# Kernel tuning notes

Hardware: AMD Instinct MI355X
Metric: run time of the kernel (lower is better)

## Reference

```python
import jax, jax.numpy as jnp
import numpy as np

N = 50000        # nodes
DEG = 32         # in-degree per node
E = N * DEG      # edges
T = 4            # towers
NODE = 128       # node_dim
OUT = 128        # out_dim
IN_T = NODE // T   # 32, divide_input tower slice
OUT_T = OUT // T   # 32
AVG_D_LOG = float(np.log(5.0))  # avg_d = {'log': log(4+1)}
EPS = 1e-5


def setup_inputs() -> dict:
    key = jax.random.key(0)
    ks = jax.random.split(key, 6)
    h = jax.random.normal(ks[0], (N, NODE), jnp.float32)
    src = jax.random.randint(ks[1], (E,), 0, N)
    # every node gets exactly DEG incoming edges (sorted dst)
    dst = jnp.repeat(jnp.arange(N), DEG)
    # per-tower pretrans MLP (1 layer): Linear(2*IN_T -> OUT_T)
    W_pre = jax.random.normal(ks[2], (T, 2 * IN_T, OUT_T), jnp.float32) * 0.05
    b_pre = jnp.zeros((T, OUT_T), jnp.float32)
    # per-tower posttrans MLP (1 layer): Linear(12*OUT_T + IN_T -> OUT_T)
    W_post = jax.random.normal(ks[3], (T, 12 * OUT_T + IN_T, OUT_T), jnp.float32) * 0.05
    b_post = jnp.zeros((T, OUT_T), jnp.float32)
    # mixing network: Linear(OUT -> OUT) + LeakyReLU
    W_mix = jax.random.normal(ks[4], (OUT, OUT), jnp.float32) * 0.05
    b_mix = jnp.zeros((OUT,), jnp.float32)
    return dict(h=h, src=src, dst=dst, W_pre=W_pre, b_pre=b_pre,
                W_post=W_post, b_post=b_post, W_mix=W_mix, b_mix=b_mix)


def _pna_forward(h, src, dst, W_pre, b_pre, W_post, b_post, W_mix, b_mix):
    ht = h.reshape(N, T, IN_T)                    # divide_input: tower slices
    z2 = jnp.concatenate([ht[src], ht[dst]], axis=-1)   # [E,T,2*IN_T] (src||dst)
    # pretrans: MLP(1 layer) then ReLU
    e = jax.nn.relu(jnp.einsum('etk,tko->eto', z2, W_pre) + b_pre)  # [E,T,OUT_T]

    deg = jax.ops.segment_sum(jnp.ones((E,), h.dtype), dst, num_segments=N)  # [N]
    deg_c = jnp.maximum(deg, 1.0)[:, None, None]
    seg = lambda x: jax.ops.segment_sum(x, dst, num_segments=N)
    mean = seg(e) / deg_c                          # [N,T,OUT_T]
    mean_sq = seg(e * e) / deg_c
    std = jnp.sqrt(jax.nn.relu(mean_sq - mean * mean) + EPS)
    mx = jax.ops.segment_max(e, dst, num_segments=N)
    mn = jax.ops.segment_min(e, dst, num_segments=N)
    agg = jnp.concatenate([mean, mx, mn, std], axis=-1)   # [N,T,4*OUT_T]

    # scalers: identity, amplification, attenuation (D = in-degree)
    sc = jnp.log(deg + 1.0) / AVG_D_LOG            # [N]
    amp = agg * sc[:, None, None]
    att = agg / jnp.maximum(sc, EPS)[:, None, None]
    h_agg = jnp.concatenate([agg, amp, att], axis=-1)     # [N,T,12*OUT_T]

    # posttrans: cat(h_tower, aggregated) -> MLP(1 layer) -> ReLU
    z = jnp.concatenate([ht, h_agg], axis=-1)      # [N,T,IN_T+12*OUT_T]
    hp = jax.nn.relu(jnp.einsum('ntk,tko->nto', z, W_post) + b_post)  # [N,T,OUT_T]
    h_cat = hp.reshape(N, OUT)

    h_out = jax.nn.leaky_relu(h_cat @ W_mix + b_mix, 0.01)
    return h + h_out                               # residual (node_dim == out_dim)


def reference(h, src, dst, W_pre, b_pre, W_post, b_post, W_mix, b_mix):
    return _pna_forward(h, src, dst, W_pre, b_pre, W_post, b_post, W_mix, b_mix)
```

## Files before the change

kernel.cpp:

```cpp
#include <hip/hip_runtime.h>
#include <hip/hip_bf16.h>
#include <math.h>

#define N_NODES 50000
#define DEG     32
#define NBF     16
#define EPSV    1e-5f

typedef __attribute__((ext_vector_type(8))) short short8;
typedef __attribute__((ext_vector_type(4))) float f32x4;
typedef __attribute__((ext_vector_type(2))) float f32x2;

__global__ void k_prep(const float* __restrict__ W_post, const float* __restrict__ W_mix,
                       const float* __restrict__ W_pre,
                       __hip_bfloat16* __restrict__ WeffT, __hip_bfloat16* __restrict__ WmixT,
                       __hip_bfloat16* __restrict__ WpreT, float sc, float isc) {
    int i = blockIdx.x * 256 + threadIdx.x;
    if (i < 20480) {
        int k = i % 160, to = i / 160, o = to & 31, t = to >> 5;
        const float* Wt = W_post + t * 416 * 32;
        float v;
        if (k < 32) v = Wt[k * 32 + o];
        else {
            int g = k - 32;
            v = Wt[(32 + g) * 32 + o] + sc * Wt[(160 + g) * 32 + o] + isc * Wt[(288 + g) * 32 + o];
        }
        WeffT[i] = __float2bfloat16(v);
    } else if (i < 36864) {
        int j = i - 20480;
        int k = j & 127, o = j >> 7;
        WmixT[j] = __float2bfloat16(W_mix[k * 128 + o]);
    } else if (i < 45056) {
        int q = i - 36864;
        int k = q & 31, o = (q >> 5) & 31, p = q >> 10;
        int t = p >> 1, half = p & 1;
        WpreT[q] = __float2bfloat16(W_pre[t * 2048 + (half * 32 + k) * 32 + o]);
    }
}

__global__ __launch_bounds__(256) void k_proj(const float* __restrict__ h,
        const __hip_bfloat16* __restrict__ WpreT, const float* __restrict__ b_pre,
        __hip_bfloat16* __restrict__ Pd, __hip_bfloat16* __restrict__ Ps) {
    __shared__ __align__(16) __hip_bfloat16 sA[64][136];
    int tid = threadIdx.x, w = tid >> 6, lane = tid & 63;
    int nb = blockIdx.x * 64;

    int colc = (tid & 31) * 4, rowb = tid >> 5;
#pragma unroll
    for (int i = 0; i < 8; ++i) {
        int row = i * 8 + rowb;
        int n = nb + row;
        unsigned int lo = 0, hi = 0;
        if (n < N_NODES) {
            float4 f = *(const float4*)(h + n * 128 + colc);
            lo = (unsigned int)__bfloat16_as_ushort(__float2bfloat16(f.x)) |
                 ((unsigned int)__bfloat16_as_ushort(__float2bfloat16(f.y)) << 16);
            hi = (unsigned int)__bfloat16_as_ushort(__float2bfloat16(f.z)) |
                 ((unsigned int)__bfloat16_as_ushort(__float2bfloat16(f.w)) << 16);
        }
        *(uint2*)(&sA[row][colc]) = make_uint2(lo, hi);
    }
    __syncthreads();

    int col = lane & 15, quad = lane >> 4;
    int r0 = w * 16;
    short8 a[4];
#pragma unroll
    for (int t = 0; t < 4; ++t)
        a[t] = *(const short8*)(&sA[r0 + col][t * 32 + quad * 8]);

#pragma unroll
    for (int p = 0; p < 8; ++p) {
        int t = p >> 1, isPd = p & 1;
#pragma unroll
        for (int ct = 0; ct < 2; ++ct) {
            int o = ct * 16 + col;
            short8 b = *(const short8*)(WpreT + p * 1024 + o * 32 + quad * 8);
            f32x4 acc = {0.f, 0.f, 0.f, 0.f};
            acc = __builtin_amdgcn_mfma_f32_16x16x32_bf16(a[t], b, acc, 0, 0, 0);
            float bp = isPd ? b_pre[t * 32 + o] : 0.f;
            __hip_bfloat16* dst = (isPd ? Pd : Ps);
#pragma unroll
            for (int r = 0; r < 4; ++r) {
                int n = nb + r0 + quad * 4 + r;
                if (n < N_NODES)
                    dst[n * 128 + t * 32 + o] = __float2bfloat16(acc[r] + bp);
            }
        }
    }
}

__global__ __launch_bounds__(256) void k_fused(const float* __restrict__ h,
        const int* __restrict__ src, const __hip_bfloat16* __restrict__ Pd,
        const __hip_bfloat16* __restrict__ Ps, const __hip_bfloat16* __restrict__ WeffT,
        const __hip_bfloat16* __restrict__ WmixT, const float* __restrict__ b_post,
        const float* __restrict__ b_mix, float* __restrict__ out) {
    __shared__ __align__(16) __hip_bfloat16 sZ[NBF][648];
    __shared__ __align__(16) __hip_bfloat16 sHp[NBF][136];
    int tid = threadIdx.x, w = tid >> 6, lane = tid & 63;
    int nb = blockIdx.x * NBF;

    int c0 = 2 * lane;
    int tA = c0 >> 5, oA = c0 & 31;
    const f32x2 zero2 = {0.f, 0.f};
#pragma unroll
    for (int r = 0; r < 4; ++r) {
        int row = r * 4 + w;
        int n = nb + row;
        int vsrc = src[n * DEG + (lane & 31)];
        float2 hv = *(const float2*)(h + n * 128 + c0);
        unsigned int pdu = *(const unsigned int*)(Pd + n * 128 + c0);
        f32x2 pd2 = {__uint_as_float(pdu << 16), __uint_as_float(pdu & 0xffff0000u)};
        f32x2 sum = zero2, sq = zero2;
        f32x2 mx = {-1e30f, -1e30f}, mn = {1e30f, 1e30f};
#pragma unroll
        for (int j0 = 0; j0 < DEG; j0 += 16) {
            unsigned int pv[16];
#pragma unroll
            for (int u = 0; u < 16; ++u) {
                int s = __builtin_amdgcn_readlane(vsrc, j0 + u);
                pv[u] = *(const unsigned int*)(Ps + s * 128 + c0);
            }
#pragma unroll
            for (int u = 0; u < 16; ++u) {
                f32x2 f = {__uint_as_float(pv[u] << 16),
                           __uint_as_float(pv[u] & 0xffff0000u)};
                f32x2 e = __builtin_elementwise_max(f + pd2, zero2);
                sum += e;
                sq = e * e + sq;
                mx = __builtin_elementwise_max(mx, e);
                mn = __builtin_elementwise_min(mn, e);
            }
        }
        f32x2 mean = sum * (1.f / DEG);
        f32x2 var = sq * (1.f / DEG) - mean * mean;
        float sd0 = sqrtf(fmaxf(var.x, 0.f) + EPSV);
        float sd1 = sqrtf(fmaxf(var.y, 0.f) + EPSV);
        unsigned int* zr = (unsigned int*)(&sZ[row][tA * 160 + oA]);
        auto pack = [](float a, float b) {
            return (unsigned int)(__bfloat16_as_ushort(__float2bfloat16(a))) |
                   ((unsigned int)(__bfloat16_as_ushort(__float2bfloat16(b))) << 16);
        };
        zr[0]  = pack(hv.x, hv.y);
        zr[16] = pack(mean.x, mean.y);
        zr[32] = pack(mx.x, mx.y);
        zr[48] = pack(mn.x, mn.y);
        zr[64] = pack(sd0, sd1);
    }
    __syncthreads();

    int col = lane & 15, quad = lane >> 4;
#pragma unroll
    for (int i = 0; i < 2; ++i) {
        int ct = w * 2 + i, t = ct >> 1, nt = ct & 1;
        f32x4 acc = {0.f, 0.f, 0.f, 0.f};
        int oc = t * 32 + nt * 16 + col;
        const __hip_bfloat16* wrow = WeffT + oc * 160 + quad * 8;
#pragma unroll
        for (int ks = 0; ks < 5; ++ks) {
            short8 a = *(const short8*)(&sZ[col][t * 160 + ks * 32 + quad * 8]);
            short8 b = *(const short8*)(wrow + ks * 32);
            acc = __builtin_amdgcn_mfma_f32_16x16x32_bf16(a, b, acc, 0, 0, 0);
        }
        float bp = b_post[oc];
#pragma unroll
        for (int r = 0; r < 4; ++r)
            sHp[quad * 4 + r][oc] = __float2bfloat16(fmaxf(acc[r] + bp, 0.f));
    }
    __syncthreads();

#pragma unroll
    for (int i = 0; i < 2; ++i) {
        int nt = w * 2 + i;
        f32x4 acc = {0.f, 0.f, 0.f, 0.f};
        int oc = nt * 16 + col;
        const __hip_bfloat16* wrow = WmixT + oc * 128 + quad * 8;
#pragma unroll
        for (int ks = 0; ks < 4; ++ks) {
            short8 a = *(const short8*)(&sHp[col][ks * 32 + quad * 8]);
            short8 b = *(const short8*)(wrow + ks * 32);
            acc = __builtin_amdgcn_mfma_f32_16x16x32_bf16(a, b, acc, 0, 0, 0);
        }
        float bm = b_mix[oc];
#pragma unroll
        for (int r = 0; r < 4; ++r) {
            int n = nb + quad * 4 + r;
            float m = acc[r] + bm;
            m = m > 0.f ? m : 0.01f * m;
            out[n * 128 + oc] = h[n * 128 + oc] + m;
        }
    }
}

extern "C" void kernel_launch(void* const* d_in, const int* in_sizes, int n_in,
                              void* d_out, int out_size, void* d_ws, size_t ws_size,
                              hipStream_t stream) {
    const float* h      = (const float*)d_in[0];
    const int*   src    = (const int*)d_in[1];
    const float* W_pre  = (const float*)d_in[3];
    const float* b_pre  = (const float*)d_in[4];
    const float* W_post = (const float*)d_in[5];
    const float* b_post = (const float*)d_in[6];
    const float* W_mix  = (const float*)d_in[7];
    const float* b_mix  = (const float*)d_in[8];
    float* out = (float*)d_out;

    char* ws = (char*)d_ws;
    __hip_bfloat16* WeffT = (__hip_bfloat16*)ws;
    __hip_bfloat16* WmixT = (__hip_bfloat16*)(ws + 40960);
    __hip_bfloat16* WpreT = (__hip_bfloat16*)(ws + 73728);
    __hip_bfloat16* Pd    = (__hip_bfloat16*)(ws + 90112);
    __hip_bfloat16* Ps    = (__hip_bfloat16*)(ws + 90112 + 12800000);

    double scd = log(33.0) / log(5.0);
    float sc = (float)scd, isc = (float)(1.0 / scd);

    hipLaunchKernelGGL(k_prep, dim3(176), dim3(256), 0, stream,
                       W_post, W_mix, W_pre, WeffT, WmixT, WpreT, sc, isc);
    hipLaunchKernelGGL(k_proj, dim3((N_NODES + 63) / 64), dim3(256), 0, stream,
                       h, WpreT, b_pre, Pd, Ps);
    hipLaunchKernelGGL(k_fused, dim3(N_NODES / NBF), dim3(256), 0, stream,
                       h, src, Pd, Ps, WeffT, WmixT, b_post, b_mix, out);
}
```

Measured before the change: 171.6 us.

## Switch edge projections to fp16 with packed half aggregation, fold prep into proj

Stores the per-node projections Pd and Ps as fp16 instead of bf16 and runs the edge aggregation (add, relu, sum, sum of squares, max, min) with packed half2 arithmetic. Each lane now covers four channels, so the neighbour gather is 8 bytes per load and half the lanes serve a second node. The separate weight-prep launch is folded into the projection kernel, which now converts W_pre on the fly and writes its output through shared memory as coalesced 16-byte stores. The aim is fewer launches, fewer ALU instructions per edge and wider memory transactions, at the cost of accumulating sums and squares in fp16, which can lose precision or overflow.

```diff
diff --git a/kernel.cpp b/kernel.cpp
--- a/kernel.cpp
+++ b/kernel.cpp
@@ -1,5 +1,6 @@
 #include <hip/hip_runtime.h>
 #include <hip/hip_bf16.h>
+#include <hip/hip_fp16.h>
 #include <math.h>
 
 #define N_NODES 50000
@@ -9,90 +10,103 @@
 
 typedef __attribute__((ext_vector_type(8))) short short8;
 typedef __attribute__((ext_vector_type(4))) float f32x4;
-typedef __attribute__((ext_vector_type(2))) float f32x2;
-
-__global__ void k_prep(const float* __restrict__ W_post, const float* __restrict__ W_mix,
-                       const float* __restrict__ W_pre,
-                       __hip_bfloat16* __restrict__ WeffT, __hip_bfloat16* __restrict__ WmixT,
-                       __hip_bfloat16* __restrict__ WpreT, float sc, float isc) {
-    int i = blockIdx.x * 256 + threadIdx.x;
-    if (i < 20480) {
-        int k = i % 160, to = i / 160, o = to & 31, t = to >> 5;
-        const float* Wt = W_post + t * 416 * 32;
-        float v;
-        if (k < 32) v = Wt[k * 32 + o];
-        else {
-            int g = k - 32;
-            v = Wt[(32 + g) * 32 + o] + sc * Wt[(160 + g) * 32 + o] + isc * Wt[(288 + g) * 32 + o];
-        }
-        WeffT[i] = __float2bfloat16(v);
-    } else if (i < 36864) {
-        int j = i - 20480;
-        int k = j & 127, o = j >> 7;
-        WmixT[j] = __float2bfloat16(W_mix[k * 128 + o]);
-    } else if (i < 45056) {
-        int q = i - 36864;
-        int k = q & 31, o = (q >> 5) & 31, p = q >> 10;
-        int t = p >> 1, half = p & 1;
-        WpreT[q] = __float2bfloat16(W_pre[t * 2048 + (half * 32 + k) * 32 + o]);
-    }
+typedef __attribute__((ext_vector_type(2))) _Float16 h16x2;
+typedef __attribute__((ext_vector_type(4))) unsigned int uint4v;
+
+__device__ __forceinline__ unsigned int bfpack(float a, float b) {
+    return (unsigned int)__bfloat16_as_ushort(__float2bfloat16(a)) |
+           ((unsigned int)__bfloat16_as_ushort(__float2bfloat16(b)) << 16);
 }
 
 __global__ __launch_bounds__(256) void k_proj(const float* __restrict__ h,
-        const __hip_bfloat16* __restrict__ WpreT, const float* __restrict__ b_pre,
-        __hip_bfloat16* __restrict__ Pd, __hip_bfloat16* __restrict__ Ps) {
-    __shared__ __align__(16) __hip_bfloat16 sA[64][136];
+        const float* __restrict__ W_pre, const float* __restrict__ b_pre,
+        const float* __restrict__ W_post, const float* __restrict__ W_mix,
+        __hip_bfloat16* __restrict__ WeffT, __hip_bfloat16* __restrict__ WmixT,
+        _Float16* __restrict__ Pd, _Float16* __restrict__ Ps, float sc, float isc) {
     int tid = threadIdx.x, w = tid >> 6, lane = tid & 63;
     int nb = blockIdx.x * 64;
 
+    if (blockIdx.x < 144) {
+        int i = blockIdx.x * 256 + tid;
+        if (i < 20480) {
+            int k = i % 160, to = i / 160, o = to & 31, t = to >> 5;
+            const float* Wt = W_post + t * 416 * 32;
+            float v;
+            if (k < 32) v = Wt[k * 32 + o];
+            else {
+                int g = k - 32;
+                v = Wt[(32 + g) * 32 + o] + sc * Wt[(160 + g) * 32 + o]
+                  + isc * Wt[(288 + g) * 32 + o];
+            }
+            WeffT[i] = __float2bfloat16(v);
+        } else {
+            int j = i - 20480;
+            int k = j & 127, o = j >> 7;
+            WmixT[j] = __float2bfloat16(W_mix[k * 128 + o]);
+        }
+    }
+
+    __shared__ __align__(16) __hip_bfloat16 sA[64][136];
     int colc = (tid & 31) * 4, rowb = tid >> 5;
 #pragma unroll
     for (int i = 0; i < 8; ++i) {
-        int row = i * 8 + rowb;
-        int n = nb + row;
+        int row = i * 8 + rowb, n = nb + row;
         unsigned int lo = 0, hi = 0;
         if (n < N_NODES) {
             float4 f = *(const float4*)(h + n * 128 + colc);
-            lo = (unsigned int)__bfloat16_as_ushort(__float2bfloat16(f.x)) |
-                 ((unsigned int)__bfloat16_as_ushort(__float2bfloat16(f.y)) << 16);
-            hi = (unsigned int)__bfloat16_as_ushort(__float2bfloat16(f.z)) |
-                 ((unsigned int)__bfloat16_as_ushort(__float2bfloat16(f.w)) << 16);
+            lo = bfpack(f.x, f.y); hi = bfpack(f.z, f.w);
         }
         *(uint2*)(&sA[row][colc]) = make_uint2(lo, hi);
     }
     __syncthreads();
-
-    int col = lane & 15, quad = lane >> 4;
-    int r0 = w * 16;
+    int col = lane & 15, quad = lane >> 4, r0 = w * 16;
     short8 a[4];
 #pragma unroll
     for (int t = 0; t < 4; ++t)
         a[t] = *(const short8*)(&sA[r0 + col][t * 32 + quad * 8]);
-
-#pragma unroll
-    for (int p = 0; p < 8; ++p) {
-        int t = p >> 1, isPd = p & 1;
-#pragma unroll
-        for (int ct = 0; ct < 2; ++ct) {
-            int o = ct * 16 + col;
-            short8 b = *(const short8*)(WpreT + p * 1024 + o * 32 + quad * 8);
-            f32x4 acc = {0.f, 0.f, 0.f, 0.f};
-            acc = __builtin_amdgcn_mfma_f32_16x16x32_bf16(a[t], b, acc, 0, 0, 0);
-            float bp = isPd ? b_pre[t * 32 + o] : 0.f;
-            __hip_bfloat16* dst = (isPd ? Pd : Ps);
-#pragma unroll
-            for (int r = 0; r < 4; ++r) {
-                int n = nb + r0 + quad * 4 + r;
-                if (n < N_NODES)
-                    dst[n * 128 + t * 32 + o] = __float2bfloat16(acc[r] + bp);
-            }
-        }
+    __syncthreads();
+    unsigned short* sOut = (unsigned short*)sA;
+
+#pragma unroll
+    for (int half = 0; half < 2; ++half) {
+#pragma unroll
+        for (int t = 0; t < 4; ++t) {
+#pragma unroll
+            for (int ct = 0; ct < 2; ++ct) {
+                int o = ct * 16 + col;
+                const float* wp = W_pre + t * 2048 + (half * 32 + quad * 8) * 32 + o;
+                unsigned int bw0 = bfpack(wp[0],   wp[32]);
+                unsigned int bw1 = bfpack(wp[64],  wp[96]);
+                unsigned int bw2 = bfpack(wp[128], wp[160]);
+                unsigned int bw3 = bfpack(wp[192], wp[224]);
+                uint4v bwv = {bw0, bw1, bw2, bw3};
+                short8 b = __builtin_bit_cast(short8, bwv);
+                f32x4 acc = {0.f, 0.f, 0.f, 0.f};
+                acc = __builtin_amdgcn_mfma_f32_16x16x32_bf16(a[t], b, acc, 0, 0, 0);
+                float bp = half ? b_pre[t * 32 + o] : 0.f;
+#pragma unroll
+                for (int r = 0; r < 4; ++r)
+                    sOut[(r0 + quad * 4 + r) * 136 + t * 32 + o] =
+                        __half_as_ushort(__float2half(acc[r] + bp));
+            }
+        }
+        __syncthreads();
+        _Float16* dst = half ? Pd : Ps;
+#pragma unroll
+        for (int rr = 0; rr < 4; ++rr) {
+            int chunk = rr * 256 + tid;
+            int row = chunk >> 4, seg = chunk & 15, n = nb + row;
+            if (n < N_NODES)
+                *(uint4v*)(dst + n * 128 + seg * 8) =
+                    *(const uint4v*)(&sOut[row * 136 + seg * 8]);
+        }
+        __syncthreads();
     }
 }
 
 __global__ __launch_bounds__(256) void k_fused(const float* __restrict__ h,
-        const int* __restrict__ src, const __hip_bfloat16* __restrict__ Pd,
-        const __hip_bfloat16* __restrict__ Ps, const __hip_bfloat16* __restrict__ WeffT,
+        const int* __restrict__ src, const _Float16* __restrict__ Pd,
+        const _Float16* __restrict__ Ps, const __hip_bfloat16* __restrict__ WeffT,
         const __hip_bfloat16* __restrict__ WmixT, const float* __restrict__ b_post,
         const float* __restrict__ b_mix, float* __restrict__ out) {
     __shared__ __align__(16) __hip_bfloat16 sZ[NBF][648];
@@ -100,52 +114,59 @@
     int tid = threadIdx.x, w = tid >> 6, lane = tid & 63;
     int nb = blockIdx.x * NBF;
 
-    int c0 = 2 * lane;
-    int tA = c0 >> 5, oA = c0 & 31;
-    const f32x2 zero2 = {0.f, 0.f};
-#pragma unroll
-    for (int r = 0; r < 4; ++r) {
-        int row = r * 4 + w;
+    int lid = lane & 31, hsel = lane & 32;
+    int cq = lid * 4;
+    int tA = cq >> 5, oA = cq & 31;
+    const h16x2 zeroh = {(_Float16)0.f, (_Float16)0.f};
+    const h16x2 bigh  = {(_Float16)65504.f, (_Float16)65504.f};
+#pragma unroll
+    for (int it = 0; it < 2; ++it) {
+        int row = it * 8 + w + (hsel >> 3);
         int n = nb + row;
-        int vsrc = src[n * DEG + (lane & 31)];
-        float2 hv = *(const float2*)(h + n * 128 + c0);
-        unsigned int pdu = *(const unsigned int*)(Pd + n * 128 + c0);
-        f32x2 pd2 = {__uint_as_float(pdu << 16), __uint_as_float(pdu & 0xffff0000u)};
-        f32x2 sum = zero2, sq = zero2;
-        f32x2 mx = {-1e30f, -1e30f}, mn = {1e30f, 1e30f};
+        int vsrc = src[n * DEG + lid];
+        float4 hv = *(const float4*)(h + n * 128 + cq);
+        uint2 pdu = *(const uint2*)(Pd + n * 128 + cq);
+        h16x2 pd01 = __builtin_bit_cast(h16x2, pdu.x);
+        h16x2 pd23 = __builtin_bit_cast(h16x2, pdu.y);
+        h16x2 sum01 = zeroh, sum23 = zeroh, sq01 = zeroh, sq23 = zeroh;
+        h16x2 mx01 = zeroh, mx23 = zeroh;
+        h16x2 mn01 = bigh, mn23 = bigh;
 #pragma unroll
         for (int j0 = 0; j0 < DEG; j0 += 16) {
-            unsigned int pv[16];
+            uint2 pv[16];
 #pragma unroll
             for (int u = 0; u < 16; ++u) {
-                int s = __builtin_amdgcn_readlane(vsrc, j0 + u);
-                pv[u] = *(const unsigned int*)(Ps + s * 128 + c0);
+                int s = __shfl(vsrc, (j0 + u) | hsel);
+                pv[u] = *(const uint2*)(Ps + s * 128 + cq);
             }
 #pragma unroll
             for (int u = 0; u < 16; ++u) {
-                f32x2 f = {__uint_as_float(pv[u] << 16),
-                           __uint_as_float(pv[u] & 0xffff0000u)};
-                f32x2 e = __builtin_elementwise_max(f + pd2, zero2);
-                sum += e;
-                sq = e * e + sq;
-                mx = __builtin_elementwise_max(mx, e);
-                mn = __builtin_elementwise_min(mn, e);
-            }
-        }
-        f32x2 mean = sum * (1.f / DEG);
-        f32x2 var = sq * (1.f / DEG) - mean * mean;
-        float sd0 = sqrtf(fmaxf(var.x, 0.f) + EPSV);
-        float sd1 = sqrtf(fmaxf(var.y, 0.f) + EPSV);
+                h16x2 f01 = __builtin_bit_cast(h16x2, pv[u].x);
+                h16x2 f23 = __builtin_bit_cast(h16x2, pv[u].y);
+                h16x2 e01 = __builtin_elementwise_max(f01 + pd01, zeroh);
+                h16x2 e23 = __builtin_elementwise_max(f23 + pd23, zeroh);
+                sum01 += e01; sq01 = e01 * e01 + sq01;
+                mx01 = __builtin_elementwise_max(mx01, e01);
+                mn01 = __builtin_elementwise_min(mn01, e01);
+                sum23 += e23; sq23 = e23 * e23 + sq23;
+                mx23 = __builtin_elementwise_max(mx23, e23);
+                mn23 = __builtin_elementwise_min(mn23, e23);
+            }
+        }
+        float mean0 = (float)sum01.x * (1.f / DEG), mean1 = (float)sum01.y * (1.f / DEG);
+        float mean2 = (float)sum23.x * (1.f / DEG), mean3 = (float)sum23.y * (1.f / DEG);
+        float sd0 = sqrtf(fmaxf((float)sq01.x * (1.f / DEG) - mean0 * mean0, 0.f) + EPSV);
+        float sd1 = sqrtf(fmaxf((float)sq01.y * (1.f / DEG) - mean1 * mean1, 0.f) + EPSV);
+        float sd2 = sqrtf(fmaxf((float)sq23.x * (1.f / DEG) - mean2 * mean2, 0.f) + EPSV);
+        float sd3 = sqrtf(fmaxf((float)sq23.y * (1.f / DEG) - mean3 * mean3, 0.f) + EPSV);
         unsigned int* zr = (unsigned int*)(&sZ[row][tA * 160 + oA]);
-        auto pack = [](float a, float b) {
-            return (unsigned int)(__bfloat16_as_ushort(__float2bfloat16(a))) |
-                   ((unsigned int)(__bfloat16_as_ushort(__float2bfloat16(b))) << 16);
-        };
-        zr[0]  = pack(hv.x, hv.y);
-        zr[16] = pack(mean.x, mean.y);
-        zr[32] = pack(mx.x, mx.y);
-        zr[48] = pack(mn.x, mn.y);
-        zr[64] = pack(sd0, sd1);
+        zr[0]  = bfpack(hv.x, hv.y);               zr[1]  = bfpack(hv.z, hv.w);
+        zr[16] = bfpack(mean0, mean1);             zr[17] = bfpack(mean2, mean3);
+        zr[32] = bfpack((float)mx01.x, (float)mx01.y);
+        zr[33] = bfpack((float)mx23.x, (float)mx23.y);
+        zr[48] = bfpack((float)mn01.x, (float)mn01.y);
+        zr[49] = bfpack((float)mn23.x, (float)mn23.y);
+        zr[64] = bfpack(sd0, sd1);                 zr[65] = bfpack(sd2, sd3);
     }
     __syncthreads();
 
@@ -208,17 +229,14 @@
     char* ws = (char*)d_ws;
     __hip_bfloat16* WeffT = (__hip_bfloat16*)ws;
     __hip_bfloat16* WmixT = (__hip_bfloat16*)(ws + 40960);
-    __hip_bfloat16* WpreT = (__hip_bfloat16*)(ws + 73728);
-    __hip_bfloat16* Pd    = (__hip_bfloat16*)(ws + 90112);
-    __hip_bfloat16* Ps    = (__hip_bfloat16*)(ws + 90112 + 12800000);
+    _Float16*       Pd    = (_Float16*)(ws + 81920);
+    _Float16*       Ps    = (_Float16*)(ws + 81920 + 12800000);
 
     double scd = log(33.0) / log(5.0);
     float sc = (float)scd, isc = (float)(1.0 / scd);
 
-    hipLaunchKernelGGL(k_prep, dim3(176), dim3(256), 0, stream,
-                       W_post, W_mix, W_pre, WeffT, WmixT, WpreT, sc, isc);
     hipLaunchKernelGGL(k_proj, dim3((N_NODES + 63) / 64), dim3(256), 0, stream,
-                       h, WpreT, b_pre, Pd, Ps);
+                       h, W_pre, b_pre, W_post, W_mix, WeffT, WmixT, Pd, Ps, sc, isc);
     hipLaunchKernelGGL(k_fused, dim3(N_NODES / NBF), dim3(256), 0, stream,
                        h, src, Pd, Ps, WeffT, WmixT, b_post, b_mix, out);
 }
```

New measurement: 164.4 us. -4.2%, faster.
